# Kernel tuning notes

Measured on AMD Instinct MI355X. Metric: run time of the kernel, lower is better.

Reference implementation:

```python
import jax, jax.numpy as jnp
import numpy as np
from jax import lax

EPS = 1e-5


def _conv3x3(x, w):
    # NCHW input, OIHW weight, stride 1, padding 1
    return lax.conv_general_dilated(
        x, w, window_strides=(1, 1), padding=((1, 1), (1, 1)),
        dimension_numbers=("NCHW", "OIHW", "NCHW"))


def _batchnorm(y, gamma, beta):
    # training-mode BN: batch statistics over N,H,W
    mean = jnp.mean(y, axis=(0, 2, 3), keepdims=True)
    var = jnp.var(y, axis=(0, 2, 3), keepdims=True)
    inv = lax.rsqrt(var + EPS)
    return (y - mean) * inv * gamma[None, :, None, None] + beta[None, :, None, None]


def setup_inputs() -> dict:
    key = jax.random.key(0)
    k1, k2, k3 = jax.random.split(key, 3)
    N, C, H, W = 32, 128, 56, 56
    x = jax.random.normal(k1, (N, C, H, W), dtype=jnp.float32)
    w1 = jax.random.normal(k2, (C, C, 3, 3), dtype=jnp.float32) * 0.05
    w2 = jax.random.normal(k3, (C, C, 3, 3), dtype=jnp.float32) * 0.05
    gamma1 = jnp.ones((C,), jnp.float32)
    beta1 = jnp.zeros((C,), jnp.float32)
    gamma2 = jnp.ones((C,), jnp.float32)
    beta2 = jnp.zeros((C,), jnp.float32)
    return {"x": x, "w1": w1, "gamma1": gamma1, "beta1": beta1,
            "w2": w2, "gamma2": gamma2, "beta2": beta2}


def reference(x, w1, gamma1, beta1, w2, gamma2, beta2):
    # binarized conv weights: sign(w), with straight-through estimator
    # (matches torch's .data swap, which routes grads to the original weight)
    w1b = w1 + lax.stop_gradient(jnp.sign(w1) - w1)
    w2b = w2 + lax.stop_gradient(jnp.sign(w2) - w2)
    out = jax.nn.relu(_batchnorm(_conv3x3(x, w1b), gamma1, beta1))
    out = _batchnorm(_conv3x3(out, w2b), gamma2, beta2)
    out = out + x  # identity shortcut (stride=1, in_planes==planes)
    return jax.nn.relu(out)
```

## Files before the change

kernel.cpp:

```cpp
#include <hip/hip_runtime.h>

typedef unsigned short u16;
typedef unsigned short u16x8 __attribute__((ext_vector_type(8)));
typedef __bf16 bf16x8 __attribute__((ext_vector_type(8)));
typedef float f32x4 __attribute__((ext_vector_type(4)));

#define HW 3136
#define NPIX 100352
#define PADR 3364
#define KD 1152

__device__ __forceinline__ float bf2f(u16 u) {
    unsigned int x = ((unsigned int)u) << 16;
    return __builtin_bit_cast(float, x);
}
__device__ __forceinline__ u16 f2bf(float f) {
    unsigned int u = __builtin_bit_cast(unsigned int, f);
    return (u16)((u + 0x7FFFu + ((u >> 16) & 1u)) >> 16);
}
__device__ __forceinline__ void gload16(const void* g, void* l) {
    __builtin_amdgcn_global_load_lds(
        (const __attribute__((address_space(1))) unsigned int*)g,
        (__attribute__((address_space(3))) unsigned int*)l, 16, 0, 0);
}

__global__ void setup_kernel(const float* __restrict__ w1, const float* __restrict__ w2,
                             u16* __restrict__ Bm1, u16* __restrict__ Bm2,
                             u16* __restrict__ xbp) {
    const int b = blockIdx.x;
    const int t = threadIdx.x;
    if (b < 1152) {
        const float* w = (b < 576) ? w1 : w2;
        u16* Bm = (b < 576) ? Bm1 : Bm2;
        int i = (b % 576) * 256 + t;
        int k  = i / KD;
        int kk = i - k * KD;
        int c  = kk & 127;
        int rs = kk >> 7;
        float v = w[(size_t)(k * 128 + c) * 9 + rs];
        float sv = (v > 0.f) ? 1.f : ((v < 0.f) ? -1.f : 0.f);
        Bm[i] = f2bf(sv);
    } else {
        int idx = (b - 1152) * 256 + t;
        int pix = idx >> 4;
        int cc  = idx & 15;
        int n  = pix / 228;
        int pb = pix - n * 228;
        int h, w;
        if (pb < 58)       { h = 0;  w = pb; }
        else if (pb < 116) { h = 57; w = pb - 58; }
        else { int q = pb - 116; h = 1 + (q >> 1); w = (q & 1) ? 57 : 0; }
        u16x8 z = {};
        *(u16x8*)(xbp + ((size_t)(n * PADR + h * 58 + w)) * 128 + cc * 8) = z;
    }
}

__global__ void x_to_nhwc(const float* __restrict__ x, u16* __restrict__ xbp) {
    __shared__ float tile[32][65];
    const int t = threadIdx.x;
    const int n = blockIdx.y;
    const int ct = blockIdx.x & 3;
    const int pt = blockIdx.x >> 2;
    const int c0 = ct * 32, p0 = pt * 64;
    {
        const int c  = t >> 3;
        const int pw = (t & 7) * 8;
        const size_t ib = ((size_t)(n * 128 + c0 + c)) * HW + p0 + pw;
        const float4 v0 = *(const float4*)(x + ib);
        const float4 v1 = *(const float4*)(x + ib + 4);
        tile[c][pw + 0] = v0.x; tile[c][pw + 1] = v0.y;
        tile[c][pw + 2] = v0.z; tile[c][pw + 3] = v0.w;
        tile[c][pw + 4] = v1.x; tile[c][pw + 5] = v1.y;
        tile[c][pw + 6] = v1.z; tile[c][pw + 7] = v1.w;
    }
    __syncthreads();
    {
        const int pl = t >> 2;
        const int cs = (t & 3) * 8;
        const int p  = p0 + pl;
        const int h  = p / 56;
        const int w  = p - h * 56;
        u16x8 o;
#pragma unroll
        for (int j = 0; j < 8; ++j) o[j] = f2bf(tile[cs + j][pl]);
        *(u16x8*)(xbp + ((size_t)(n * PADR + (h + 1) * 58 + (w + 1))) * 128 + c0 + cs) = o;
    }
}

__global__ __launch_bounds__(256, 4) void conv_mfma(
    const u16* __restrict__ xbp, const u16* __restrict__ Bm,
    u16* __restrict__ y, float2* __restrict__ partial)
{
    __shared__ __align__(16) u16 smem[20480];
    u16* As = smem;
    u16* Bs = smem + 8192;
    const int t = threadIdx.x;
    const int bid = blockIdx.x;
    const int pm0 = bid * 128;
    const int wid  = t >> 6;
    const int lane = t & 63;
    const int lrow = lane & 15;
    const int lhk  = lane >> 4;
    const int m0 = (wid >> 1) * 64;
    const int n0 = (wid & 1) * 64;

    const int rsub = lane >> 3;
    const int csrc = (lane & 7) ^ rsub;
    int apix[4], bbase[4];
#pragma unroll
    for (int j = 0; j < 4; ++j) {
        int row = (wid * 4 + j) * 8 + rsub;
        int ps  = pm0 + row;
        int n   = ps / HW;
        int rem = ps - n * HW;
        int h   = rem / 56;
        int w   = rem - h * 56;
        apix[j]  = (n * PADR + (h + 1) * 58 + (w + 1)) * 128 + csrc * 8;
        bbase[j] = row * KD + csrc * 8;
    }

    f32x4 acc[4][4] = {};

#pragma unroll 1
    for (int pp = 0; pp < 18; ++pp) {
        const int rs_ = pp >> 1;
        const int r_ = rs_ / 3, s_ = rs_ - r_ * 3;
        const int ash = ((r_ - 1) * 58 + (s_ - 1)) * 128 + (pp & 1) * 64;
        const int bsh = pp * 64;
#pragma unroll
        for (int j = 0; j < 4; ++j) {
            gload16(xbp + apix[j] + ash, As + (wid * 4 + j) * 512);
            gload16(Bm + bbase[j] + bsh, Bs + (wid * 4 + j) * 512);
        }
        __syncthreads();
#pragma unroll
        for (int kc = 0; kc < 2; ++kc) {
            bf16x8 af[4], bv[4];
#pragma unroll
            for (int mi = 0; mi < 4; ++mi) {
                int ck = (((kc << 2) | lhk) ^ (lrow & 7)) << 3;
                af[mi] = *(const bf16x8*)&As[(m0 + mi * 16 + lrow) * 64 + ck];
            }
#pragma unroll
            for (int ni = 0; ni < 4; ++ni) {
                int ck = (((kc << 2) | lhk) ^ (lrow & 7)) << 3;
                bv[ni] = *(const bf16x8*)&Bs[(n0 + ni * 16 + lrow) * 64 + ck];
            }
#pragma unroll
            for (int mi = 0; mi < 4; ++mi)
#pragma unroll
                for (int ni = 0; ni < 4; ++ni)
                    acc[mi][ni] = __builtin_amdgcn_mfma_f32_16x16x32_bf16(
                        af[mi], bv[ni], acc[mi][ni], 0, 0, 0);
        }
        __syncthreads();
    }

    float sv[4], qv[4];
#pragma unroll
    for (int ni = 0; ni < 4; ++ni) {
        float a = 0.f, b = 0.f;
#pragma unroll
        for (int mi = 0; mi < 4; ++mi)
#pragma unroll
            for (int q = 0; q < 4; ++q) { float v = acc[mi][ni][q]; a += v; b += v * v; }
        a += __shfl_xor(a, 16); a += __shfl_xor(a, 32);
        b += __shfl_xor(b, 16); b += __shfl_xor(b, 32);
        sv[ni] = a; qv[ni] = b;
    }
    float2* sred = (float2*)(smem + 17408);
    if (lane < 16) {
#pragma unroll
        for (int ni = 0; ni < 4; ++ni)
            sred[wid * 64 + ni * 16 + lane] = make_float2(sv[ni], qv[ni]);
    }

#pragma unroll
    for (int mi = 0; mi < 4; ++mi)
#pragma unroll
        for (int ni = 0; ni < 4; ++ni)
#pragma unroll
            for (int q = 0; q < 4; ++q)
                smem[(m0 + mi * 16 + lhk * 4 + q) * 136 + n0 + ni * 16 + lrow] =
                    f2bf(acc[mi][ni][q]);
    __syncthreads();
    {
        const int px = t >> 1, half = t & 1;
        const u16* src = &smem[px * 136 + half * 64];
        u16* dst = y + (size_t)(pm0 + px) * 128 + half * 64;
#pragma unroll
        for (int j = 0; j < 8; ++j)
            *(u16x8*)(dst + j * 8) = *(const u16x8*)(src + j * 8);
    }
    if (t < 128) {
        const int ni = (t >> 4) & 3, oc = t & 15, hi = t >> 6;
        float2 u = sred[hi * 64 + ni * 16 + oc];
        float2 v = sred[(hi + 2) * 64 + ni * 16 + oc];
        partial[(size_t)t * 784 + bid] = make_float2(u.x + v.x, u.y + v.y);
    }
}

__global__ void stats_finalize(const float2* __restrict__ partial,
                               const float* __restrict__ gamma, const float* __restrict__ beta,
                               float2* __restrict__ coef) {
    __shared__ float ss[256], ss2[256];
    const int c = blockIdx.x, t = threadIdx.x;
    const float2* pc = partial + (size_t)c * 784;
    float s = 0.f, s2 = 0.f;
    for (int i = t; i < 784; i += 256) { float2 v = pc[i]; s += v.x; s2 += v.y; }
    ss[t] = s; ss2[t] = s2;
    __syncthreads();
    for (int o = 128; o > 0; o >>= 1) {
        if (t < o) { ss[t] += ss[t + o]; ss2[t] += ss2[t + o]; }
        __syncthreads();
    }
    if (t == 0) {
        double mean = (double)ss[0] / (double)NPIX;
        double var  = (double)ss2[0] / (double)NPIX - mean * mean;
        if (var < 0.0) var = 0.0;
        float inv = rsqrtf((float)var + 1e-5f);
        float a = gamma[c] * inv;
        coef[c] = make_float2(a, beta[c] - (float)mean * a);
    }
}

__global__ void bnrelu_kernel(const u16* __restrict__ y, const float2* __restrict__ coef,
                              u16* __restrict__ out1p) {
    __shared__ float2 sc[128];
    const int b = blockIdx.x;
    const int t = threadIdx.x;
    if (b >= 6272) {
        int idx = (b - 6272) * 256 + t;
        int pix = idx >> 4;
        int cc  = idx & 15;
        int n  = pix / 228;
        int pb = pix - n * 228;
        int h, w;
        if (pb < 58)       { h = 0;  w = pb; }
        else if (pb < 116) { h = 57; w = pb - 58; }
        else { int q = pb - 116; h = 1 + (q >> 1); w = (q & 1) ? 57 : 0; }
        u16x8 z = {};
        *(u16x8*)(out1p + ((size_t)(n * PADR + h * 58 + w)) * 128 + cc * 8) = z;
        return;
    }
    if (t < 128) sc[t] = coef[t];
    __syncthreads();
    size_t i = (size_t)b * 256 + t;
    u16x8 v = *(const u16x8*)(y + i * 8);
    int p  = (int)(i >> 4);
    int c0 = (int)(i & 15) * 8;
    int n   = p / HW;
    int rem = p - n * HW;
    int h   = rem / 56;
    int w   = rem - h * 56;
    u16x8 o;
#pragma unroll
    for (int j = 0; j < 8; ++j) {
        float2 k = sc[c0 + j];
        o[j] = f2bf(fmaxf(bf2f(v[j]) * k.x + k.y, 0.f));
    }
    *(u16x8*)(out1p + ((size_t)(n * PADR + (h + 1) * 58 + (w + 1))) * 128 + c0) = o;
}

__global__ void bn_add_relu_nchw(const u16* __restrict__ y2, const float2* __restrict__ coef,
                                 const u16* __restrict__ xbp, float* __restrict__ out) {
    __shared__ float tile[32][65];
    __shared__ float2 sc[32];
    const int t = threadIdx.x;
    const int n = blockIdx.y;
    const int ct = blockIdx.x & 3;
    const int pt = blockIdx.x >> 2;
    const int c0 = ct * 32, p0 = pt * 64;
    if (t < 32) sc[t] = coef[c0 + t];
    __syncthreads();
    {
        const int pl = t >> 2;
        const int cs = (t & 3) * 8;
        const int p  = p0 + pl;
        const int h  = p / 56;
        const int w  = p - h * 56;
        const u16x8 v = *(const u16x8*)(y2 + ((size_t)(n * HW + p)) * 128 + c0 + cs);
        const u16x8 xv = *(const u16x8*)(xbp +
            ((size_t)(n * PADR + (h + 1) * 58 + (w + 1))) * 128 + c0 + cs);
#pragma unroll
        for (int j = 0; j < 8; ++j) {
            float2 k = sc[cs + j];
            tile[cs + j][pl] = bf2f(v[j]) * k.x + k.y + bf2f(xv[j]);
        }
    }
    __syncthreads();
    {
        const int c  = t >> 3;
        const int pw = (t & 7) * 8;
        const size_t ob = ((size_t)(n * 128 + c0 + c)) * HW + p0 + pw;
        float4 o0, o1;
        o0.x = fmaxf(tile[c][pw + 0], 0.f);
        o0.y = fmaxf(tile[c][pw + 1], 0.f);
        o0.z = fmaxf(tile[c][pw + 2], 0.f);
        o0.w = fmaxf(tile[c][pw + 3], 0.f);
        o1.x = fmaxf(tile[c][pw + 4], 0.f);
        o1.y = fmaxf(tile[c][pw + 5], 0.f);
        o1.z = fmaxf(tile[c][pw + 6], 0.f);
        o1.w = fmaxf(tile[c][pw + 7], 0.f);
        *(float4*)(out + ob) = o0;
        *(float4*)(out + ob + 4) = o1;
    }
}

extern "C" void kernel_launch(void* const* d_in, const int* in_sizes, int n_in,
                              void* d_out, int out_size, void* d_ws, size_t ws_size,
                              hipStream_t stream) {
    const float* x  = (const float*)d_in[0];
    const float* w1 = (const float*)d_in[1];
    const float* g1 = (const float*)d_in[2];
    const float* b1 = (const float*)d_in[3];
    const float* w2 = (const float*)d_in[4];
    const float* g2 = (const float*)d_in[5];
    const float* b2 = (const float*)d_in[6];
    float* out = (float*)d_out;
    char* ws = (char*)d_ws;

    u16*    xbp   = (u16*)(ws);
    u16*    ybuf  = (u16*)(ws + 27557888);
    u16*    Bm1   = (u16*)(ws + 53248000);
    u16*    Bm2   = (u16*)(ws + 53542912);
    float2* part  = (float2*)(ws + 53837824);
    float2* cf1   = (float2*)(ws + 54640640);
    float2* cf2   = (float2*)(ws + 54641664);
    u16*    out1p = (u16*)d_out;

    setup_kernel<<<1608, 256, 0, stream>>>(w1, w2, Bm1, Bm2, xbp);
    x_to_nhwc<<<dim3(196, 32), 256, 0, stream>>>(x, xbp);

    conv_mfma<<<784, 256, 0, stream>>>(xbp, Bm1, ybuf, part);
    stats_finalize<<<128, 256, 0, stream>>>(part, g1, b1, cf1);
    bnrelu_kernel<<<6728, 256, 0, stream>>>(ybuf, cf1, out1p);

    conv_mfma<<<784, 256, 0, stream>>>(out1p, Bm2, ybuf, part);
    stats_finalize<<<128, 256, 0, stream>>>(part, g2, b2, cf2);
    bn_add_relu_nchw<<<dim3(196, 32), 256, 0, stream>>>(ybuf, cf2, xbp, out);
}
```

Before: 147.0 us.

## Use 2-wave conv blocks with 128x64 warp tiles and swizzled block order

The conv kernel drops from four waves per block to two. Each wave now computes a 128x64 output tile (8x4 MFMA tiles) instead of 64x64, so every wave reuses the full A tile and register pressure roughly doubles. Block indices are also permuted in groups of 8, likely to spread neighbouring tiles across XCDs or improve cache locality. The cost is fewer waves per CU and per block for hiding latency, and each thread issues twice as many loads.

```diff
diff --git a/kernel.cpp b/kernel.cpp
--- a/kernel.cpp
+++ b/kernel.cpp
@@ -87,29 +87,28 @@
     }
 }
 
-__global__ __launch_bounds__(256, 4) void conv_mfma(
+__global__ __launch_bounds__(128, 2) void conv_mfma(
     const u16* __restrict__ xbp, const u16* __restrict__ Bm,
     u16* __restrict__ y, float2* __restrict__ partial)
 {
-    __shared__ __align__(16) u16 smem[20480];
-    u16* As = smem;
-    u16* Bs = smem + 8192;
-    const int t = threadIdx.x;
-    const int bid = blockIdx.x;
+    __shared__ __align__(16) u16 smem[18432];
+    const int t = threadIdx.x;
+    const int bid0 = blockIdx.x;
+    const int bid = (bid0 & 7) * 98 + (bid0 >> 3);
     const int pm0 = bid * 128;
     const int wid  = t >> 6;
     const int lane = t & 63;
     const int lrow = lane & 15;
     const int lhk  = lane >> 4;
-    const int m0 = (wid >> 1) * 64;
-    const int n0 = (wid & 1) * 64;
+    const int n0   = wid * 64;
 
     const int rsub = lane >> 3;
     const int csrc = (lane & 7) ^ rsub;
-    int apix[4], bbase[4];
-#pragma unroll
-    for (int j = 0; j < 4; ++j) {
-        int row = (wid * 4 + j) * 8 + rsub;
+    int apix[8], bbase[8];
+#pragma unroll
+    for (int j = 0; j < 8; ++j) {
+        int g   = wid * 8 + j;
+        int row = g * 8 + rsub;
         int ps  = pm0 + row;
         int n   = ps / HW;
         int rem = ps - n * HW;
@@ -119,7 +118,7 @@
         bbase[j] = row * KD + csrc * 8;
     }
 
-    f32x4 acc[4][4] = {};
+    f32x4 acc[8][4] = {};
 
 #pragma unroll 1
     for (int pp = 0; pp < 18; ++pp) {
@@ -128,26 +127,24 @@
         const int ash = ((r_ - 1) * 58 + (s_ - 1)) * 128 + (pp & 1) * 64;
         const int bsh = pp * 64;
 #pragma unroll
-        for (int j = 0; j < 4; ++j) {
-            gload16(xbp + apix[j] + ash, As + (wid * 4 + j) * 512);
-            gload16(Bm + bbase[j] + bsh, Bs + (wid * 4 + j) * 512);
+        for (int j = 0; j < 8; ++j) {
+            const int g = wid * 8 + j;
+            gload16(xbp + apix[j] + ash, smem + g * 512);
+            gload16(Bm + bbase[j] + bsh, smem + 8192 + g * 512);
         }
         __syncthreads();
 #pragma unroll
         for (int kc = 0; kc < 2; ++kc) {
-            bf16x8 af[4], bv[4];
-#pragma unroll
-            for (int mi = 0; mi < 4; ++mi) {
-                int ck = (((kc << 2) | lhk) ^ (lrow & 7)) << 3;
-                af[mi] = *(const bf16x8*)&As[(m0 + mi * 16 + lrow) * 64 + ck];
-            }
-#pragma unroll
-            for (int ni = 0; ni < 4; ++ni) {
-                int ck = (((kc << 2) | lhk) ^ (lrow & 7)) << 3;
-                bv[ni] = *(const bf16x8*)&Bs[(n0 + ni * 16 + lrow) * 64 + ck];
-            }
-#pragma unroll
-            for (int mi = 0; mi < 4; ++mi)
+            const int ck = (((kc << 2) | lhk) ^ (lrow & 7)) << 3;
+            bf16x8 af[8], bv[4];
+#pragma unroll
+            for (int mi = 0; mi < 8; ++mi)
+                af[mi] = *(const bf16x8*)&smem[(mi * 16 + lrow) * 64 + ck];
+#pragma unroll
+            for (int ni = 0; ni < 4; ++ni)
+                bv[ni] = *(const bf16x8*)&smem[8192 + (n0 + ni * 16 + lrow) * 64 + ck];
+#pragma unroll
+            for (int mi = 0; mi < 8; ++mi)
 #pragma unroll
                 for (int ni = 0; ni < 4; ++ni)
                     acc[mi][ni] = __builtin_amdgcn_mfma_f32_16x16x32_bf16(
@@ -156,47 +153,43 @@
         __syncthreads();
     }
 
-    float sv[4], qv[4];
-#pragma unroll
-    for (int ni = 0; ni < 4; ++ni) {
-        float a = 0.f, b = 0.f;
-#pragma unroll
-        for (int mi = 0; mi < 4; ++mi)
-#pragma unroll
-            for (int q = 0; q < 4; ++q) { float v = acc[mi][ni][q]; a += v; b += v * v; }
-        a += __shfl_xor(a, 16); a += __shfl_xor(a, 32);
-        b += __shfl_xor(b, 16); b += __shfl_xor(b, 32);
-        sv[ni] = a; qv[ni] = b;
-    }
     float2* sred = (float2*)(smem + 17408);
-    if (lane < 16) {
+    {
+        float sv[4], qv[4];
+#pragma unroll
+        for (int ni = 0; ni < 4; ++ni) {
+            float a = 0.f, b = 0.f;
+#pragma unroll
+            for (int mi = 0; mi < 8; ++mi)
+#pragma unroll
+                for (int q = 0; q < 4; ++q) { float v = acc[mi][ni][q]; a += v; b += v * v; }
+            a += __shfl_xor(a, 16); a += __shfl_xor(a, 32);
+            b += __shfl_xor(b, 16); b += __shfl_xor(b, 32);
+            sv[ni] = a; qv[ni] = b;
+        }
+        if (lane < 16) {
+#pragma unroll
+            for (int ni = 0; ni < 4; ++ni)
+                sred[n0 + ni * 16 + lane] = make_float2(sv[ni], qv[ni]);
+        }
+    }
+
+#pragma unroll
+    for (int mi = 0; mi < 8; ++mi)
 #pragma unroll
         for (int ni = 0; ni < 4; ++ni)
-            sred[wid * 64 + ni * 16 + lane] = make_float2(sv[ni], qv[ni]);
-    }
-
-#pragma unroll
-    for (int mi = 0; mi < 4; ++mi)
-#pragma unroll
-        for (int ni = 0; ni < 4; ++ni)
 #pragma unroll
             for (int q = 0; q < 4; ++q)
-                smem[(m0 + mi * 16 + lhk * 4 + q) * 136 + n0 + ni * 16 + lrow] =
+                smem[(mi * 16 + lhk * 4 + q) * 136 + n0 + ni * 16 + lrow] =
                     f2bf(acc[mi][ni][q]);
     __syncthreads();
     {
-        const int px = t >> 1, half = t & 1;
-        const u16* src = &smem[px * 136 + half * 64];
-        u16* dst = y + (size_t)(pm0 + px) * 128 + half * 64;
-#pragma unroll
-        for (int j = 0; j < 8; ++j)
+        const u16* src = &smem[t * 136];
+        u16* dst = y + (size_t)(pm0 + t) * 128;
+#pragma unroll
+        for (int j = 0; j < 16; ++j)
             *(u16x8*)(dst + j * 8) = *(const u16x8*)(src + j * 8);
-    }
-    if (t < 128) {
-        const int ni = (t >> 4) & 3, oc = t & 15, hi = t >> 6;
-        float2 u = sred[hi * 64 + ni * 16 + oc];
-        float2 v = sred[(hi + 2) * 64 + ni * 16 + oc];
-        partial[(size_t)t * 784 + bid] = make_float2(u.x + v.x, u.y + v.y);
+        partial[(size_t)t * 784 + bid] = sred[t];
     }
 }
 
@@ -332,11 +325,11 @@
     setup_kernel<<<1608, 256, 0, stream>>>(w1, w2, Bm1, Bm2, xbp);
     x_to_nhwc<<<dim3(196, 32), 256, 0, stream>>>(x, xbp);
 
-    conv_mfma<<<784, 256, 0, stream>>>(xbp, Bm1, ybuf, part);
+    conv_mfma<<<784, 128, 0, stream>>>(xbp, Bm1, ybuf, part);
     stats_finalize<<<128, 256, 0, stream>>>(part, g1, b1, cf1);
     bnrelu_kernel<<<6728, 256, 0, stream>>>(ybuf, cf1, out1p);
 
-    conv_mfma<<<784, 256, 0, stream>>>(out1p, Bm2, ybuf, part);
+    conv_mfma<<<784, 128, 0, stream>>>(out1p, Bm2, ybuf, part);
     stats_finalize<<<128, 256, 0, stream>>>(part, g2, b2, cf2);
     bn_add_relu_nchw<<<dim3(196, 32), 256, 0, stream>>>(ybuf, cf2, xbp, out);
 }
```

After: 152.4 us. 3.6% more time.

## Balance conv grid to 768 blocks with tail pixels spread as extra work

Applied to the files above, without the earlier changes.

Cuts the conv grid from 784 to 768 blocks of 128 pixels. The remaining 2048 pixels are split into 64 small 32-pixel tiles, each computed by every twelfth block after its main tile, so the wave count fits the CU count better (256 CUs × 3 = 768). Block ids are also remapped so consecutive launched blocks touch pixel tiles spaced apart, likely to spread XCD/L2 locality. The cost is extra serial work and syncs in some blocks, which may create stragglers. The partial-stat buffer widens to 832 slots.

```diff
diff --git a/kernel.cpp b/kernel.cpp
--- a/kernel.cpp
+++ b/kernel.cpp
@@ -9,6 +9,8 @@
 #define NPIX 100352
 #define PADR 3364
 #define KD 1152
+#define NBLK 768
+#define NSLOT 832
 
 __device__ __forceinline__ float bf2f(u16 u) {
     unsigned int x = ((unsigned int)u) << 16;
@@ -95,7 +97,8 @@
     u16* As = smem;
     u16* Bs = smem + 8192;
     const int t = threadIdx.x;
-    const int bid = blockIdx.x;
+    const int bid0 = blockIdx.x;
+    const int bid = (bid0 & 7) * 96 + (bid0 >> 3);
     const int pm0 = bid * 128;
     const int wid  = t >> 6;
     const int lane = t & 63;
@@ -156,23 +159,25 @@
         __syncthreads();
     }
 
-    float sv[4], qv[4];
-#pragma unroll
-    for (int ni = 0; ni < 4; ++ni) {
-        float a = 0.f, b = 0.f;
-#pragma unroll
-        for (int mi = 0; mi < 4; ++mi)
-#pragma unroll
-            for (int q = 0; q < 4; ++q) { float v = acc[mi][ni][q]; a += v; b += v * v; }
-        a += __shfl_xor(a, 16); a += __shfl_xor(a, 32);
-        b += __shfl_xor(b, 16); b += __shfl_xor(b, 32);
-        sv[ni] = a; qv[ni] = b;
-    }
     float2* sred = (float2*)(smem + 17408);
-    if (lane < 16) {
-#pragma unroll
-        for (int ni = 0; ni < 4; ++ni)
-            sred[wid * 64 + ni * 16 + lane] = make_float2(sv[ni], qv[ni]);
+    {
+        float sv[4], qv[4];
+#pragma unroll
+        for (int ni = 0; ni < 4; ++ni) {
+            float a = 0.f, b = 0.f;
+#pragma unroll
+            for (int mi = 0; mi < 4; ++mi)
+#pragma unroll
+                for (int q = 0; q < 4; ++q) { float v = acc[mi][ni][q]; a += v; b += v * v; }
+            a += __shfl_xor(a, 16); a += __shfl_xor(a, 32);
+            b += __shfl_xor(b, 16); b += __shfl_xor(b, 32);
+            sv[ni] = a; qv[ni] = b;
+        }
+        if (lane < 16) {
+#pragma unroll
+            for (int ni = 0; ni < 4; ++ni)
+                sred[wid * 64 + ni * 16 + lane] = make_float2(sv[ni], qv[ni]);
+        }
     }
 
 #pragma unroll
@@ -196,7 +201,91 @@
         const int ni = (t >> 4) & 3, oc = t & 15, hi = t >> 6;
         float2 u = sred[hi * 64 + ni * 16 + oc];
         float2 v = sred[(hi + 2) * 64 + ni * 16 + oc];
-        partial[(size_t)t * 784 + bid] = make_float2(u.x + v.x, u.y + v.y);
+        partial[(size_t)t * NSLOT + bid] = make_float2(u.x + v.x, u.y + v.y);
+    }
+
+    if ((bid % 12) == 0 && (bid / 12) < 64) {
+        const int e = bid / 12;
+        const int ppix0 = 98304 + e * 32;
+        __syncthreads();
+
+        int apixE;
+        {
+            int row = wid * 8 + rsub;
+            int ps  = ppix0 + row;
+            int n   = ps / HW;
+            int rem = ps - n * HW;
+            int h   = rem / 56;
+            int w   = rem - h * 56;
+            apixE = (n * PADR + (h + 1) * 58 + (w + 1)) * 128 + csrc * 8;
+        }
+        const int m0E = (wid >> 1) * 16;
+        f32x4 acc2[4] = {};
+
+#pragma unroll 1
+        for (int pp = 0; pp < 18; ++pp) {
+            const int rs_ = pp >> 1;
+            const int r_ = rs_ / 3, s_ = rs_ - r_ * 3;
+            const int ash = ((r_ - 1) * 58 + (s_ - 1)) * 128 + (pp & 1) * 64;
+            const int bsh = pp * 64;
+            gload16(xbp + apixE + ash, As + wid * 512);
+#pragma unroll
+            for (int j = 0; j < 4; ++j)
+                gload16(Bm + bbase[j] + bsh, Bs + (wid * 4 + j) * 512);
+            __syncthreads();
+#pragma unroll
+            for (int kc = 0; kc < 2; ++kc) {
+                const int ck = (((kc << 2) | lhk) ^ (lrow & 7)) << 3;
+                bf16x8 afE = *(const bf16x8*)&As[(m0E + lrow) * 64 + ck];
+                bf16x8 bv[4];
+#pragma unroll
+                for (int ni = 0; ni < 4; ++ni)
+                    bv[ni] = *(const bf16x8*)&Bs[(n0 + ni * 16 + lrow) * 64 + ck];
+#pragma unroll
+                for (int ni = 0; ni < 4; ++ni)
+                    acc2[ni] = __builtin_amdgcn_mfma_f32_16x16x32_bf16(
+                        afE, bv[ni], acc2[ni], 0, 0, 0);
+            }
+            __syncthreads();
+        }
+
+        {
+            float sv[4], qv[4];
+#pragma unroll
+            for (int ni = 0; ni < 4; ++ni) {
+                float a = 0.f, b = 0.f;
+#pragma unroll
+                for (int q = 0; q < 4; ++q) { float v = acc2[ni][q]; a += v; b += v * v; }
+                a += __shfl_xor(a, 16); a += __shfl_xor(a, 32);
+                b += __shfl_xor(b, 16); b += __shfl_xor(b, 32);
+                sv[ni] = a; qv[ni] = b;
+            }
+            if (lane < 16) {
+#pragma unroll
+                for (int ni = 0; ni < 4; ++ni)
+                    sred[wid * 64 + ni * 16 + lane] = make_float2(sv[ni], qv[ni]);
+            }
+        }
+#pragma unroll
+        for (int ni = 0; ni < 4; ++ni)
+#pragma unroll
+            for (int q = 0; q < 4; ++q)
+                smem[(m0E + lhk * 4 + q) * 136 + n0 + ni * 16 + lrow] = f2bf(acc2[ni][q]);
+        __syncthreads();
+        {
+            const int px = t >> 3;
+            const int off = (t & 7) * 16;
+            u16* dst = y + (size_t)(ppix0 + px) * 128 + off;
+            const u16* src = &smem[px * 136 + off];
+            *(u16x8*)(dst)     = *(const u16x8*)(src);
+            *(u16x8*)(dst + 8) = *(const u16x8*)(src + 8);
+        }
+        if (t < 128) {
+            const int ni = (t >> 4) & 3, oc = t & 15, hi = t >> 6;
+            float2 u = sred[hi * 64 + ni * 16 + oc];
+            float2 v = sred[(hi + 2) * 64 + ni * 16 + oc];
+            partial[(size_t)t * NSLOT + NBLK + e] = make_float2(u.x + v.x, u.y + v.y);
+        }
     }
 }
 
@@ -205,9 +294,9 @@
                                float2* __restrict__ coef) {
     __shared__ float ss[256], ss2[256];
     const int c = blockIdx.x, t = threadIdx.x;
-    const float2* pc = partial + (size_t)c * 784;
+    const float2* pc = partial + (size_t)c * NSLOT;
     float s = 0.f, s2 = 0.f;
-    for (int i = t; i < 784; i += 256) { float2 v = pc[i]; s += v.x; s2 += v.y; }
+    for (int i = t; i < NSLOT; i += 256) { float2 v = pc[i]; s += v.x; s2 += v.y; }
     ss[t] = s; ss2[t] = s2;
     __syncthreads();
     for (int o = 128; o > 0; o >>= 1) {
@@ -325,18 +414,18 @@
     u16*    Bm1   = (u16*)(ws + 53248000);
     u16*    Bm2   = (u16*)(ws + 53542912);
     float2* part  = (float2*)(ws + 53837824);
-    float2* cf1   = (float2*)(ws + 54640640);
-    float2* cf2   = (float2*)(ws + 54641664);
+    float2* cf1   = (float2*)(ws + 54689792);
+    float2* cf2   = (float2*)(ws + 54690816);
     u16*    out1p = (u16*)d_out;
 
     setup_kernel<<<1608, 256, 0, stream>>>(w1, w2, Bm1, Bm2, xbp);
     x_to_nhwc<<<dim3(196, 32), 256, 0, stream>>>(x, xbp);
 
-    conv_mfma<<<784, 256, 0, stream>>>(xbp, Bm1, ybuf, part);
+    conv_mfma<<<NBLK, 256, 0, stream>>>(xbp, Bm1, ybuf, part);
     stats_finalize<<<128, 256, 0, stream>>>(part, g1, b1, cf1);
     bnrelu_kernel<<<6728, 256, 0, stream>>>(ybuf, cf1, out1p);
 
-    conv_mfma<<<784, 256, 0, stream>>>(out1p, Bm2, ybuf, part);
+    conv_mfma<<<NBLK, 256, 0, stream>>>(out1p, Bm2, ybuf, part);
     stats_finalize<<<128, 256, 0, stream>>>(part, g2, b2, cf2);
     bn_add_relu_nchw<<<dim3(196, 32), 256, 0, stream>>>(ybuf, cf2, xbp, out);
 }
```

Result: slower. 153.7 us (+4.5%).

## Fuse BN stats finalize into conv via last-block atomic counter

Applied to the files above, without the earlier changes.

Removes the separate stats_finalize launches: each conv block writes its partial sums, bumps an atomic counter, and the last block reduces all partials and computes the BN coefficients. Border zeroing of the padded out1p buffer moves from bnrelu into the setup kernel, and conv block indices are remapped so consecutive launched blocks are spread across the pixel range. This saves two launches at the cost of a serial tail reduction in a single block and extra fences.

```diff
diff --git a/kernel.cpp b/kernel.cpp
--- a/kernel.cpp
+++ b/kernel.cpp
@@ -9,6 +9,7 @@
 #define NPIX 100352
 #define PADR 3364
 #define KD 1152
+#define NBLK 784
 
 __device__ __forceinline__ float bf2f(u16 u) {
     unsigned int x = ((unsigned int)u) << 16;
@@ -26,9 +27,14 @@
 
 __global__ void setup_kernel(const float* __restrict__ w1, const float* __restrict__ w2,
                              u16* __restrict__ Bm1, u16* __restrict__ Bm2,
-                             u16* __restrict__ xbp) {
+                             u16* __restrict__ xbp, u16* __restrict__ out1p,
+                             int* __restrict__ counters) {
     const int b = blockIdx.x;
     const int t = threadIdx.x;
+    if (b == 2064) {
+        if (t < 2) counters[t] = 0;
+        return;
+    }
     if (b < 1152) {
         const float* w = (b < 576) ? w1 : w2;
         u16* Bm = (b < 576) ? Bm1 : Bm2;
@@ -41,7 +47,9 @@
         float sv = (v > 0.f) ? 1.f : ((v < 0.f) ? -1.f : 0.f);
         Bm[i] = f2bf(sv);
     } else {
-        int idx = (b - 1152) * 256 + t;
+        const bool toOut = (b >= 1608);
+        u16* dst = toOut ? out1p : xbp;
+        int idx = ((toOut ? b - 1608 : b - 1152)) * 256 + t;
         int pix = idx >> 4;
         int cc  = idx & 15;
         int n  = pix / 228;
@@ -51,7 +59,7 @@
         else if (pb < 116) { h = 57; w = pb - 58; }
         else { int q = pb - 116; h = 1 + (q >> 1); w = (q & 1) ? 57 : 0; }
         u16x8 z = {};
-        *(u16x8*)(xbp + ((size_t)(n * PADR + h * 58 + w)) * 128 + cc * 8) = z;
+        *(u16x8*)(dst + ((size_t)(n * PADR + h * 58 + w)) * 128 + cc * 8) = z;
     }
 }
 
@@ -89,13 +97,16 @@
 
 __global__ __launch_bounds__(256, 4) void conv_mfma(
     const u16* __restrict__ xbp, const u16* __restrict__ Bm,
-    u16* __restrict__ y, float2* __restrict__ partial)
+    u16* __restrict__ y, float2* __restrict__ partial,
+    const float* __restrict__ gamma, const float* __restrict__ beta,
+    float2* __restrict__ coef, int* __restrict__ counter)
 {
     __shared__ __align__(16) u16 smem[20480];
     u16* As = smem;
     u16* Bs = smem + 8192;
     const int t = threadIdx.x;
-    const int bid = blockIdx.x;
+    const int bid0 = blockIdx.x;
+    const int bid = (bid0 & 7) * 98 + (bid0 >> 3);
     const int pm0 = bid * 128;
     const int wid  = t >> 6;
     const int lane = t & 63;
@@ -156,96 +167,88 @@
         __syncthreads();
     }
 
-    float sv[4], qv[4];
-#pragma unroll
-    for (int ni = 0; ni < 4; ++ni) {
-        float a = 0.f, b = 0.f;
-#pragma unroll
-        for (int mi = 0; mi < 4; ++mi)
-#pragma unroll
-            for (int q = 0; q < 4; ++q) { float v = acc[mi][ni][q]; a += v; b += v * v; }
-        a += __shfl_xor(a, 16); a += __shfl_xor(a, 32);
-        b += __shfl_xor(b, 16); b += __shfl_xor(b, 32);
-        sv[ni] = a; qv[ni] = b;
-    }
     float2* sred = (float2*)(smem + 17408);
-    if (lane < 16) {
-#pragma unroll
-        for (int ni = 0; ni < 4; ++ni)
-            sred[wid * 64 + ni * 16 + lane] = make_float2(sv[ni], qv[ni]);
-    }
-
-#pragma unroll
-    for (int mi = 0; mi < 4; ++mi)
-#pragma unroll
-        for (int ni = 0; ni < 4; ++ni)
-#pragma unroll
-            for (int q = 0; q < 4; ++q)
-                smem[(m0 + mi * 16 + lhk * 4 + q) * 136 + n0 + ni * 16 + lrow] =
-                    f2bf(acc[mi][ni][q]);
-    __syncthreads();
-    {
-        const int px = t >> 1, half = t & 1;
-        const u16* src = &smem[px * 136 + half * 64];
-        u16* dst = y + (size_t)(pm0 + px) * 128 + half * 64;
-#pragma unroll
-        for (int j = 0; j < 8; ++j)
-            *(u16x8*)(dst + j * 8) = *(const u16x8*)(src + j * 8);
-    }
+    {
+        float sv[4], qv[4];
+#pragma unroll
+        for (int ni = 0; ni < 4; ++ni) {
+            float a = 0.f, b = 0.f;
+#pragma unroll
+            for (int mi = 0; mi < 4; ++mi)
+#pragma unroll
+                for (int q = 0; q < 4; ++q) { float v = acc[mi][ni][q]; a += v; b += v * v; }
+            a += __shfl_xor(a, 16); a += __shfl_xor(a, 32);
+            b += __shfl_xor(b, 16); b += __shfl_xor(b, 32);
+            sv[ni] = a; qv[ni] = b;
+        }
+        if (lane < 16) {
+#pragma unroll
+            for (int ni = 0; ni < 4; ++ni)
+                sred[wid * 64 + ni * 16 + lane] = make_float2(sv[ni], qv[ni]);
+        }
+    }
+    __syncthreads();
     if (t < 128) {
         const int ni = (t >> 4) & 3, oc = t & 15, hi = t >> 6;
         float2 u = sred[hi * 64 + ni * 16 + oc];
         float2 v = sred[(hi + 2) * 64 + ni * 16 + oc];
-        partial[(size_t)t * 784 + bid] = make_float2(u.x + v.x, u.y + v.y);
-    }
-}
-
-__global__ void stats_finalize(const float2* __restrict__ partial,
-                               const float* __restrict__ gamma, const float* __restrict__ beta,
-                               float2* __restrict__ coef) {
-    __shared__ float ss[256], ss2[256];
-    const int c = blockIdx.x, t = threadIdx.x;
-    const float2* pc = partial + (size_t)c * 784;
-    float s = 0.f, s2 = 0.f;
-    for (int i = t; i < 784; i += 256) { float2 v = pc[i]; s += v.x; s2 += v.y; }
-    ss[t] = s; ss2[t] = s2;
-    __syncthreads();
-    for (int o = 128; o > 0; o >>= 1) {
-        if (t < o) { ss[t] += ss[t + o]; ss2[t] += ss2[t + o]; }
+        partial[(size_t)t * NBLK + bid] = make_float2(u.x + v.x, u.y + v.y);
+    }
+    __threadfence();
+
+#pragma unroll
+    for (int mi = 0; mi < 4; ++mi)
+#pragma unroll
+        for (int ni = 0; ni < 4; ++ni)
+#pragma unroll
+            for (int q = 0; q < 4; ++q)
+                smem[(m0 + mi * 16 + lhk * 4 + q) * 136 + n0 + ni * 16 + lrow] =
+                    f2bf(acc[mi][ni][q]);
+    __syncthreads();
+    {
+        const int px = t >> 1, half = t & 1;
+        const u16* src = &smem[px * 136 + half * 64];
+        u16* dst = y + (size_t)(pm0 + px) * 128 + half * 64;
+#pragma unroll
+        for (int j = 0; j < 8; ++j)
+            *(u16x8*)(dst + j * 8) = *(const u16x8*)(src + j * 8);
+    }
+    __syncthreads();
+
+    if (t == 0) smem[0] = (atomicAdd(counter, 1) == NBLK - 1) ? 1 : 0;
+    __syncthreads();
+    if (smem[0] == 0) return;
+    __syncthreads();
+    __threadfence();
+    {
+        const int c = t >> 1;
+        const float2* pc = partial + (size_t)c * NBLK + (t & 1) * 392;
+        float s = 0.f, q = 0.f;
+        for (int i = 0; i < 392; ++i) { float2 v = pc[i]; s += v.x; q += v.y; }
+        float* fs = (float*)smem;
+        float* fq = fs + 256;
+        fs[t] = s; fq[t] = q;
         __syncthreads();
-    }
-    if (t == 0) {
-        double mean = (double)ss[0] / (double)NPIX;
-        double var  = (double)ss2[0] / (double)NPIX - mean * mean;
-        if (var < 0.0) var = 0.0;
-        float inv = rsqrtf((float)var + 1e-5f);
-        float a = gamma[c] * inv;
-        coef[c] = make_float2(a, beta[c] - (float)mean * a);
+        if (t < 128) {
+            double ss = (double)fs[2 * t] + (double)fs[2 * t + 1];
+            double qq = (double)fq[2 * t] + (double)fq[2 * t + 1];
+            double mean = ss / (double)NPIX;
+            double var  = qq / (double)NPIX - mean * mean;
+            if (var < 0.0) var = 0.0;
+            float inv = rsqrtf((float)var + 1e-5f);
+            float a = gamma[t] * inv;
+            coef[t] = make_float2(a, beta[t] - (float)mean * a);
+        }
     }
 }
 
 __global__ void bnrelu_kernel(const u16* __restrict__ y, const float2* __restrict__ coef,
                               u16* __restrict__ out1p) {
     __shared__ float2 sc[128];
-    const int b = blockIdx.x;
-    const int t = threadIdx.x;
-    if (b >= 6272) {
-        int idx = (b - 6272) * 256 + t;
-        int pix = idx >> 4;
-        int cc  = idx & 15;
-        int n  = pix / 228;
-        int pb = pix - n * 228;
-        int h, w;
-        if (pb < 58)       { h = 0;  w = pb; }
-        else if (pb < 116) { h = 57; w = pb - 58; }
-        else { int q = pb - 116; h = 1 + (q >> 1); w = (q & 1) ? 57 : 0; }
-        u16x8 z = {};
-        *(u16x8*)(out1p + ((size_t)(n * PADR + h * 58 + w)) * 128 + cc * 8) = z;
-        return;
-    }
+    const int t = threadIdx.x;
     if (t < 128) sc[t] = coef[t];
     __syncthreads();
-    size_t i = (size_t)b * 256 + t;
+    size_t i = (size_t)blockIdx.x * 256 + t;
     u16x8 v = *(const u16x8*)(y + i * 8);
     int p  = (int)(i >> 4);
     int c0 = (int)(i & 15) * 8;
@@ -327,16 +330,18 @@
     float2* part  = (float2*)(ws + 53837824);
     float2* cf1   = (float2*)(ws + 54640640);
     float2* cf2   = (float2*)(ws + 54641664);
+    int*    cnts  = (int*)(ws + 54642688);
     u16*    out1p = (u16*)d_out;
 
-    setup_kernel<<<1608, 256, 0, stream>>>(w1, w2, Bm1, Bm2, xbp);
+    int* cnt1 = cnts;
+    int* cnt2 = cnts + 1;
+
+    setup_kernel<<<2065, 256, 0, stream>>>(w1, w2, Bm1, Bm2, xbp, out1p, cnts);
     x_to_nhwc<<<dim3(196, 32), 256, 0, stream>>>(x, xbp);
 
-    conv_mfma<<<784, 256, 0, stream>>>(xbp, Bm1, ybuf, part);
-    stats_finalize<<<128, 256, 0, stream>>>(part, g1, b1, cf1);
-    bnrelu_kernel<<<6728, 256, 0, stream>>>(ybuf, cf1, out1p);
-
-    conv_mfma<<<784, 256, 0, stream>>>(out1p, Bm2, ybuf, part);
-    stats_finalize<<<128, 256, 0, stream>>>(part, g2, b2, cf2);
+    conv_mfma<<<NBLK, 256, 0, stream>>>(xbp, Bm1, ybuf, part, g1, b1, cf1, cnt1);
+    bnrelu_kernel<<<6272, 256, 0, stream>>>(ybuf, cf1, out1p);
+
+    conv_mfma<<<NBLK, 256, 0, stream>>>(out1p, Bm2, ybuf, part, g2, b2, cf2, cnt2);
     bn_add_relu_nchw<<<dim3(196, 32), 256, 0, stream>>>(ybuf, cf2, xbp, out);
 }
```

After: 358.0 us. 143% more time.
